# Performance work log

Measured on AMD Instinct MI355X. Metric: run time of the kernel, lower is better.

The kernel has to match this reference:

```python
import jax, jax.numpy as jnp
import numpy as np

COST_CLASS = 1.0
COST_BBOX = 5.0
COST_GIOU = 2.0


def box_cxcywh_to_xyxy(b):
    cx, cy, w, h = jnp.split(b, 4, axis=-1)
    return jnp.concatenate([cx - 0.5 * w, cy - 0.5 * h, cx + 0.5 * w, cy + 0.5 * h], axis=-1)


def generalized_box_iou(boxes1, boxes2):
    # boxes1: [N,4] xyxy, boxes2: [M,4] xyxy -> [N,M]
    area1 = (boxes1[:, 2] - boxes1[:, 0]) * (boxes1[:, 3] - boxes1[:, 1])
    area2 = (boxes2[:, 2] - boxes2[:, 0]) * (boxes2[:, 3] - boxes2[:, 1])
    lt = jnp.maximum(boxes1[:, None, :2], boxes2[None, :, :2])
    rb = jnp.minimum(boxes1[:, None, 2:], boxes2[None, :, 2:])
    wh = jnp.clip(rb - lt, 0.0)
    inter = wh[..., 0] * wh[..., 1]
    union = area1[:, None] + area2[None, :] - inter
    iou = inter / union
    lt_e = jnp.minimum(boxes1[:, None, :2], boxes2[None, :, :2])
    rb_e = jnp.maximum(boxes1[:, None, 2:], boxes2[None, :, 2:])
    wh_e = jnp.clip(rb_e - lt_e, 0.0)
    area_e = wh_e[..., 0] * wh_e[..., 1]
    return iou - (area_e - union) / area_e


def setup_inputs() -> dict:
    key = jax.random.key(0)
    k1, k2, k3, k4 = jax.random.split(key, 4)
    pred_logits = jax.random.normal(k1, (16, 900, 91), dtype=jnp.float32)
    pred_boxes = jax.random.uniform(k2, (16, 900, 4), dtype=jnp.float32)  # cxcywh in (0,1)
    tgt_labels = jax.random.randint(k3, (1600,), 0, 91)
    tgt_boxes = jax.random.uniform(k4, (1600, 4), dtype=jnp.float32)
    return {"pred_logits": pred_logits, "pred_boxes": pred_boxes,
            "tgt_labels": tgt_labels, "tgt_boxes": tgt_boxes}


def reference(pred_logits, pred_boxes, tgt_labels, tgt_boxes):
    bs, num_queries, _ = pred_logits.shape
    out_prob = jax.nn.softmax(pred_logits.reshape(bs * num_queries, -1), axis=-1)  # [BQ, C]
    out_bbox = pred_boxes.reshape(bs * num_queries, 4)  # [BQ, 4]
    # classification cost: -p(class=tgt)
    cost_class = -out_prob[:, tgt_labels]  # [BQ, M]
    # L1 cdist on cxcywh boxes
    cost_bbox = jnp.sum(jnp.abs(out_bbox[:, None, :] - tgt_boxes[None, :, :]), axis=-1)  # [BQ, M]
    # GIoU cost
    cost_giou = -generalized_box_iou(box_cxcywh_to_xyxy(out_bbox), box_cxcywh_to_xyxy(tgt_boxes))
    C = COST_BBOX * cost_bbox + COST_CLASS * cost_class + COST_GIOU * cost_giou
    return C.reshape(bs, num_queries, -1)  # [bs, Q, total_tgt]
```

## Files before the change

### kernel.cpp

```cpp
#include <hip/hip_runtime.h>

#define QT 8
#define NM 1600
#define NG (NM / 4)
#define NC 91
#define BLOCK 256

typedef float f32x4 __attribute__((ext_vector_type(4)));
typedef float f32x2 __attribute__((ext_vector_type(2)));

__global__ __launch_bounds__(BLOCK, 5) void matcher_cost_kernel(
    const float* __restrict__ logits,
    const float* __restrict__ pboxes,
    const int*   __restrict__ tlabels,
    const float* __restrict__ tboxes,
    float* __restrict__ out)
{
    __shared__ float4 s_cx[NG], s_cy[NG], s_hw[NG], s_hh[NG];
    __shared__ unsigned s_lab[NG];
    __shared__ float s_c2[QT][NC + 1];

    const int tid  = threadIdx.x;
    const int wv   = tid >> 6;
    const int lane = tid & 63;
    const int q0   = blockIdx.x * QT;

    const float4* tb4 = (const float4*)tboxes;
    const int4*   lb4 = (const int4*)tlabels;
    for (int g = tid; g < NG; g += BLOCK) {
        float4 t0 = tb4[4 * g + 0], t1 = tb4[4 * g + 1];
        float4 t2 = tb4[4 * g + 2], t3 = tb4[4 * g + 3];
        s_cx[g] = make_float4(t0.x, t1.x, t2.x, t3.x);
        s_cy[g] = make_float4(t0.y, t1.y, t2.y, t3.y);
        s_hw[g] = make_float4(0.5f * t0.z, 0.5f * t1.z, 0.5f * t2.z, 0.5f * t3.z);
        s_hh[g] = make_float4(0.5f * t0.w, 0.5f * t1.w, 0.5f * t2.w, 0.5f * t3.w);
        int4 vl = lb4[g];
        s_lab[g] = (unsigned)(vl.x & 0xff) | ((unsigned)(vl.y & 0xff) << 8)
                 | ((unsigned)(vl.z & 0xff) << 16) | ((unsigned)(vl.w & 0xff) << 24);
    }

    #pragma unroll
    for (int k = 0; k < 2; ++k) {
        const int ql = 2 * wv + k;
        const float* lrow = logits + (size_t)(q0 + ql) * NC;
        float v0 = (lane      < NC) ? lrow[lane]      : -3.4e38f;
        float v1 = (lane + 64 < NC) ? lrow[lane + 64] : -3.4e38f;
        float mx = fmaxf(v0, v1);
        #pragma unroll
        for (int off = 32; off; off >>= 1) mx = fmaxf(mx, __shfl_xor(mx, off));
        float e0 = (lane      < NC) ? __expf(v0 - mx) : 0.0f;
        float e1 = (lane + 64 < NC) ? __expf(v1 - mx) : 0.0f;
        float s = e0 + e1;
        #pragma unroll
        for (int off = 32; off; off >>= 1) s += __shfl_xor(s, off);
        float inv = 1.0f / s;
        if (lane      < NC) s_c2[ql][lane]      = 2.0f - e0 * inv;
        if (lane + 64 < NC) s_c2[ql][lane + 64] = 2.0f - e1 * inv;
    }

    f32x2 qcx[2], qcy[2], qhw[2], qhh[2], qa[2];
    #pragma unroll
    for (int k = 0; k < 2; ++k) {
        float4 pb = ((const float4*)pboxes)[q0 + 2 * wv + k];
        qcx[k] = (f32x2){pb.x, pb.x};
        qcy[k] = (f32x2){pb.y, pb.y};
        qhw[k] = (f32x2){0.5f * pb.z, 0.5f * pb.z};
        qhh[k] = (f32x2){0.5f * pb.w, 0.5f * pb.w};
        float a = pb.z * pb.w;
        qa[k]  = (f32x2){a, a};
    }

    __syncthreads();

    const f32x2 zero2 = {0.0f, 0.0f};

    for (int g = lane; g < NG; g += 64) {
        float4 vcx = s_cx[g], vcy = s_cy[g], vhw = s_hw[g], vhh = s_hh[g];
        unsigned labw = s_lab[g];
        f32x2 tcx[2] = {{vcx.x, vcx.y}, {vcx.z, vcx.w}};
        f32x2 tcy[2] = {{vcy.x, vcy.y}, {vcy.z, vcy.w}};
        f32x2 thw[2] = {{vhw.x, vhw.y}, {vhw.z, vhw.w}};
        f32x2 thh[2] = {{vhh.x, vhh.y}, {vhh.z, vhh.w}};
        f32x2 ta[2];
        #pragma unroll
        for (int h = 0; h < 2; ++h) ta[h] = 4.0f * (thw[h] * thh[h]);

        #pragma unroll
        for (int k = 0; k < 2; ++k) {
            const int ql = 2 * wv + k;
            const float* tab = s_c2[ql];
            f32x2 rr2[2];
            #pragma unroll
            for (int h = 0; h < 2; ++h) {
                f32x2 adx = __builtin_elementwise_abs(qcx[k] - tcx[h]);
                f32x2 ady = __builtin_elementwise_abs(qcy[k] - tcy[h]);
                f32x2 adw = __builtin_elementwise_abs(qhw[k] - thw[h]);
                f32x2 adh = __builtin_elementwise_abs(qhh[k] - thh[h]);
                f32x2 A = adx + ady;
                f32x2 B = adw + adh;
                f32x2 sx = qhw[k] + thw[h];
                f32x2 sy = qhh[k] + thh[h];
                f32x2 mxx = __builtin_elementwise_max(adx, adw);
                f32x2 mxy = __builtin_elementwise_max(ady, adh);
                f32x2 iw = __builtin_elementwise_max(sx - mxx, zero2);
                f32x2 ih = __builtin_elementwise_max(sy - mxy, zero2);
                f32x2 inter = iw * ih;
                f32x2 earea = (sx + mxx) * (sy + mxy);
                f32x2 uni = (qa[k] + ta[h]) - inter;
                f32x2 ue = uni * earea;
                f32x2 rr = {__builtin_amdgcn_rcpf(ue[0]),
                            __builtin_amdgcn_rcpf(ue[1])};
                f32x2 X = (uni * uni + inter * earea) * rr;
                f32x2 c2 = {tab[(labw >> (16 * h)) & 0xff],
                            tab[(labw >> (16 * h + 8)) & 0xff]};
                rr2[h] = -2.0f * X + (5.0f * A + (10.0f * B + c2));
            }
            f32x4 r4 = {rr2[0][0], rr2[0][1], rr2[1][0], rr2[1][1]};
            __builtin_nontemporal_store(r4,
                (f32x4*)(out + (size_t)(q0 + ql) * NM) + g);
        }
    }
}

extern "C" void kernel_launch(void* const* d_in, const int* in_sizes, int n_in,
                              void* d_out, int out_size, void* d_ws, size_t ws_size,
                              hipStream_t stream) {
    const float* logits  = (const float*)d_in[0];
    const float* pboxes  = (const float*)d_in[1];
    const int*   tlabels = (const int*)d_in[2];
    const float* tboxes  = (const float*)d_in[3];
    float* out = (float*)d_out;

    const int BQ = in_sizes[1] / 4;
    const int grid = BQ / QT;
    matcher_cost_kernel<<<grid, BLOCK, 0, stream>>>(logits, pboxes, tlabels, tboxes, out);
}
```

Measured before the change: 30.74 us.

## Make matcher kernel persistent, with waves striding over query-pair halves

Replaces the one-block-per-8-queries grid with a fixed 1280-block persistent grid. Each wave loops over work units made of a query pair and one half of the targets. This spreads the target-table staging in shared memory over many query rows and gives finer-grained load balancing. In exchange, each wave recomputes the softmax for its query pair once per half, so every logits row is processed twice, and there is no barrier between each wave's shared-table writes and its reads.

```diff
diff --git a/kernel.cpp b/kernel.cpp
--- a/kernel.cpp
+++ b/kernel.cpp
@@ -1,10 +1,11 @@
 #include <hip/hip_runtime.h>
 
-#define QT 8
 #define NM 1600
 #define NG (NM / 4)
+#define NH (NG / 2)
 #define NC 91
 #define BLOCK 256
+#define GRID 1280
 
 typedef float f32x4 __attribute__((ext_vector_type(4)));
 typedef float f32x2 __attribute__((ext_vector_type(2)));
@@ -14,16 +15,16 @@
     const float* __restrict__ pboxes,
     const int*   __restrict__ tlabels,
     const float* __restrict__ tboxes,
-    float* __restrict__ out)
+    float* __restrict__ out,
+    int BQ)
 {
     __shared__ float4 s_cx[NG], s_cy[NG], s_hw[NG], s_hh[NG];
     __shared__ unsigned s_lab[NG];
-    __shared__ float s_c2[QT][NC + 1];
+    __shared__ float s_tab[4][2][NC + 5];
 
     const int tid  = threadIdx.x;
     const int wv   = tid >> 6;
     const int lane = tid & 63;
-    const int q0   = blockIdx.x * QT;
 
     const float4* tb4 = (const float4*)tboxes;
     const int4*   lb4 = (const int4*)tlabels;
@@ -38,86 +39,93 @@
         s_lab[g] = (unsigned)(vl.x & 0xff) | ((unsigned)(vl.y & 0xff) << 8)
                  | ((unsigned)(vl.z & 0xff) << 16) | ((unsigned)(vl.w & 0xff) << 24);
     }
-
-    #pragma unroll
-    for (int k = 0; k < 2; ++k) {
-        const int ql = 2 * wv + k;
-        const float* lrow = logits + (size_t)(q0 + ql) * NC;
-        float v0 = (lane      < NC) ? lrow[lane]      : -3.4e38f;
-        float v1 = (lane + 64 < NC) ? lrow[lane + 64] : -3.4e38f;
-        float mx = fmaxf(v0, v1);
-        #pragma unroll
-        for (int off = 32; off; off >>= 1) mx = fmaxf(mx, __shfl_xor(mx, off));
-        float e0 = (lane      < NC) ? __expf(v0 - mx) : 0.0f;
-        float e1 = (lane + 64 < NC) ? __expf(v1 - mx) : 0.0f;
-        float s = e0 + e1;
-        #pragma unroll
-        for (int off = 32; off; off >>= 1) s += __shfl_xor(s, off);
-        float inv = 1.0f / s;
-        if (lane      < NC) s_c2[ql][lane]      = 2.0f - e0 * inv;
-        if (lane + 64 < NC) s_c2[ql][lane + 64] = 2.0f - e1 * inv;
-    }
-
-    f32x2 qcx[2], qcy[2], qhw[2], qhh[2], qa[2];
-    #pragma unroll
-    for (int k = 0; k < 2; ++k) {
-        float4 pb = ((const float4*)pboxes)[q0 + 2 * wv + k];
-        qcx[k] = (f32x2){pb.x, pb.x};
-        qcy[k] = (f32x2){pb.y, pb.y};
-        qhw[k] = (f32x2){0.5f * pb.z, 0.5f * pb.z};
-        qhh[k] = (f32x2){0.5f * pb.w, 0.5f * pb.w};
-        float a = pb.z * pb.w;
-        qa[k]  = (f32x2){a, a};
-    }
-
     __syncthreads();
 
+    const int npair = BQ >> 1;
+    const int totw  = (int)gridDim.x * 4;
+    const int gwid  = (int)blockIdx.x * 4 + wv;
     const f32x2 zero2 = {0.0f, 0.0f};
 
-    for (int g = lane; g < NG; g += 64) {
-        float4 vcx = s_cx[g], vcy = s_cy[g], vhw = s_hw[g], vhh = s_hh[g];
-        unsigned labw = s_lab[g];
-        f32x2 tcx[2] = {{vcx.x, vcx.y}, {vcx.z, vcx.w}};
-        f32x2 tcy[2] = {{vcy.x, vcy.y}, {vcy.z, vcy.w}};
-        f32x2 thw[2] = {{vhw.x, vhw.y}, {vhw.z, vhw.w}};
-        f32x2 thh[2] = {{vhh.x, vhh.y}, {vhh.z, vhh.w}};
-        f32x2 ta[2];
-        #pragma unroll
-        for (int h = 0; h < 2; ++h) ta[h] = 4.0f * (thw[h] * thh[h]);
+    for (int u = gwid; u < BQ; u += totw) {
+        const int half = (u >= npair) ? 1 : 0;
+        const int pair = u - half * npair;
 
         #pragma unroll
         for (int k = 0; k < 2; ++k) {
-            const int ql = 2 * wv + k;
-            const float* tab = s_c2[ql];
-            f32x2 rr2[2];
+            const int q = 2 * pair + k;
+            const float* lrow = logits + (size_t)q * NC;
+            float v0 = (lane      < NC) ? lrow[lane]      : -3.4e38f;
+            float v1 = (lane + 64 < NC) ? lrow[lane + 64] : -3.4e38f;
+            float mx = fmaxf(v0, v1);
             #pragma unroll
-            for (int h = 0; h < 2; ++h) {
-                f32x2 adx = __builtin_elementwise_abs(qcx[k] - tcx[h]);
-                f32x2 ady = __builtin_elementwise_abs(qcy[k] - tcy[h]);
-                f32x2 adw = __builtin_elementwise_abs(qhw[k] - thw[h]);
-                f32x2 adh = __builtin_elementwise_abs(qhh[k] - thh[h]);
-                f32x2 A = adx + ady;
-                f32x2 B = adw + adh;
-                f32x2 sx = qhw[k] + thw[h];
-                f32x2 sy = qhh[k] + thh[h];
-                f32x2 mxx = __builtin_elementwise_max(adx, adw);
-                f32x2 mxy = __builtin_elementwise_max(ady, adh);
-                f32x2 iw = __builtin_elementwise_max(sx - mxx, zero2);
-                f32x2 ih = __builtin_elementwise_max(sy - mxy, zero2);
-                f32x2 inter = iw * ih;
-                f32x2 earea = (sx + mxx) * (sy + mxy);
-                f32x2 uni = (qa[k] + ta[h]) - inter;
-                f32x2 ue = uni * earea;
-                f32x2 rr = {__builtin_amdgcn_rcpf(ue[0]),
-                            __builtin_amdgcn_rcpf(ue[1])};
-                f32x2 X = (uni * uni + inter * earea) * rr;
-                f32x2 c2 = {tab[(labw >> (16 * h)) & 0xff],
-                            tab[(labw >> (16 * h + 8)) & 0xff]};
-                rr2[h] = -2.0f * X + (5.0f * A + (10.0f * B + c2));
+            for (int off = 32; off; off >>= 1) mx = fmaxf(mx, __shfl_xor(mx, off));
+            float e0 = (lane      < NC) ? __expf(v0 - mx) : 0.0f;
+            float e1 = (lane + 64 < NC) ? __expf(v1 - mx) : 0.0f;
+            float s = e0 + e1;
+            #pragma unroll
+            for (int off = 32; off; off >>= 1) s += __shfl_xor(s, off);
+            float inv = 1.0f / s;
+            if (lane      < NC) s_tab[wv][k][lane]      = 2.0f - e0 * inv;
+            if (lane + 64 < NC) s_tab[wv][k][lane + 64] = 2.0f - e1 * inv;
+        }
+
+        f32x2 qcx[2], qcy[2], qhw[2], qhh[2], qa[2];
+        #pragma unroll
+        for (int k = 0; k < 2; ++k) {
+            float4 pb = ((const float4*)pboxes)[2 * pair + k];
+            qcx[k] = (f32x2){pb.x, pb.x};
+            qcy[k] = (f32x2){pb.y, pb.y};
+            qhw[k] = (f32x2){0.5f * pb.z, 0.5f * pb.z};
+            qhh[k] = (f32x2){0.5f * pb.w, 0.5f * pb.w};
+            float a = pb.z * pb.w;
+            qa[k]  = (f32x2){a, a};
+        }
+
+        const int gbeg = half * NH;
+        for (int g = gbeg + lane; g < gbeg + NH; g += 64) {
+            float4 vcx = s_cx[g], vcy = s_cy[g], vhw = s_hw[g], vhh = s_hh[g];
+            unsigned labw = s_lab[g];
+            f32x2 tcx[2] = {{vcx.x, vcx.y}, {vcx.z, vcx.w}};
+            f32x2 tcy[2] = {{vcy.x, vcy.y}, {vcy.z, vcy.w}};
+            f32x2 thw[2] = {{vhw.x, vhw.y}, {vhw.z, vhw.w}};
+            f32x2 thh[2] = {{vhh.x, vhh.y}, {vhh.z, vhh.w}};
+            f32x2 ta[2];
+            #pragma unroll
+            for (int h = 0; h < 2; ++h) ta[h] = 4.0f * (thw[h] * thh[h]);
+
+            #pragma unroll
+            for (int k = 0; k < 2; ++k) {
+                const float* tab = s_tab[wv][k];
+                f32x2 rr2[2];
+                #pragma unroll
+                for (int h = 0; h < 2; ++h) {
+                    f32x2 adx = __builtin_elementwise_abs(qcx[k] - tcx[h]);
+                    f32x2 ady = __builtin_elementwise_abs(qcy[k] - tcy[h]);
+                    f32x2 adw = __builtin_elementwise_abs(qhw[k] - thw[h]);
+                    f32x2 adh = __builtin_elementwise_abs(qhh[k] - thh[h]);
+                    f32x2 A = adx + ady;
+                    f32x2 B = adw + adh;
+                    f32x2 sx = qhw[k] + thw[h];
+                    f32x2 sy = qhh[k] + thh[h];
+                    f32x2 mxx = __builtin_elementwise_max(adx, adw);
+                    f32x2 mxy = __builtin_elementwise_max(ady, adh);
+                    f32x2 iw = __builtin_elementwise_max(sx - mxx, zero2);
+                    f32x2 ih = __builtin_elementwise_max(sy - mxy, zero2);
+                    f32x2 inter = iw * ih;
+                    f32x2 earea = (sx + mxx) * (sy + mxy);
+                    f32x2 uni = (qa[k] + ta[h]) - inter;
+                    f32x2 ue = uni * earea;
+                    f32x2 rr = {__builtin_amdgcn_rcpf(ue[0]),
+                                __builtin_amdgcn_rcpf(ue[1])};
+                    f32x2 X = (uni * uni + inter * earea) * rr;
+                    f32x2 c2 = {tab[(labw >> (16 * h)) & 0xff],
+                                tab[(labw >> (16 * h + 8)) & 0xff]};
+                    rr2[h] = -2.0f * X + (5.0f * A + (10.0f * B + c2));
+                }
+                f32x4 r4 = {rr2[0][0], rr2[0][1], rr2[1][0], rr2[1][1]};
+                __builtin_nontemporal_store(r4,
+                    (f32x4*)(out + (size_t)(2 * pair + k) * NM) + g);
             }
-            f32x4 r4 = {rr2[0][0], rr2[0][1], rr2[1][0], rr2[1][1]};
-            __builtin_nontemporal_store(r4,
-                (f32x4*)(out + (size_t)(q0 + ql) * NM) + g);
         }
     }
 }
@@ -132,6 +140,6 @@
     float* out = (float*)d_out;
 
     const int BQ = in_sizes[1] / 4;
-    const int grid = BQ / QT;
-    matcher_cost_kernel<<<grid, BLOCK, 0, stream>>>(logits, pboxes, tlabels, tboxes, out);
+    matcher_cost_kernel<<<GRID, BLOCK, 0, stream>>>(logits, pboxes, tlabels,
+                                                    tboxes, out, BQ);
 }
```

New measurement: 37.23 us. 21.1% more time.

## Split softmax into a pre-pass kernel and pack target boxes as fp16 in LDS

Applied to the files above, without the earlier changes.

Moves the per-query softmax into a separate kernel that writes 2-p values into the workspace, which the cost kernel then copies into shared memory. Stores the target box coordinates in shared memory as half2 instead of float4, halving that footprint, and raises the launch-bounds occupancy hint from 5 to 8. The aim is more resident waves to hide latency on the store-bound output write. In exchange it adds a second kernel launch and a workspace round-trip. The fp16 target coordinates also lose precision, which may exceed the accuracy tolerance.

```diff
diff --git a/kernel.cpp b/kernel.cpp
--- a/kernel.cpp
+++ b/kernel.cpp
@@ -1,24 +1,51 @@
 #include <hip/hip_runtime.h>
+#include <hip/hip_fp16.h>
 
 #define QT 8
 #define NM 1600
 #define NG (NM / 4)
 #define NC 91
+#define CSTRIDE 92
 #define BLOCK 256
 
 typedef float f32x4 __attribute__((ext_vector_type(4)));
 typedef float f32x2 __attribute__((ext_vector_type(2)));
 
-__global__ __launch_bounds__(BLOCK, 5) void matcher_cost_kernel(
+__global__ __launch_bounds__(BLOCK) void softmax_c2_kernel(
+    const float* __restrict__ logits, float* __restrict__ c2, int BQ)
+{
+    const int wv = threadIdx.x >> 6, lane = threadIdx.x & 63;
+    const int q  = blockIdx.x * 4 + wv;
+    if (q >= BQ) return;
+    const float* lrow = logits + (size_t)q * NC;
+    float v0 = (lane      < NC) ? lrow[lane]      : -3.4e38f;
+    float v1 = (lane + 64 < NC) ? lrow[lane + 64] : -3.4e38f;
+    float mx = fmaxf(v0, v1);
+    #pragma unroll
+    for (int off = 32; off; off >>= 1) mx = fmaxf(mx, __shfl_xor(mx, off));
+    float e0 = (lane      < NC) ? __expf(v0 - mx) : 0.0f;
+    float e1 = (lane + 64 < NC) ? __expf(v1 - mx) : 0.0f;
+    float s = e0 + e1;
+    #pragma unroll
+    for (int off = 32; off; off >>= 1) s += __shfl_xor(s, off);
+    float inv = 1.0f / s;
+    float* crow = c2 + (size_t)q * CSTRIDE;
+    if (lane      < NC) crow[lane]      = 2.0f - e0 * inv;
+    if (lane + 64 < NC) crow[lane + 64] = 2.0f - e1 * inv;
+}
+
+template <bool USE_WS>
+__global__ __launch_bounds__(BLOCK, 8) void matcher_cost_kernel(
     const float* __restrict__ logits,
     const float* __restrict__ pboxes,
     const int*   __restrict__ tlabels,
     const float* __restrict__ tboxes,
+    const float* __restrict__ c2g,
     float* __restrict__ out)
 {
-    __shared__ float4 s_cx[NG], s_cy[NG], s_hw[NG], s_hh[NG];
+    __shared__ __half2 s_cx[NG][2], s_cy[NG][2], s_hw[NG][2], s_hh[NG][2];
     __shared__ unsigned s_lab[NG];
-    __shared__ float s_c2[QT][NC + 1];
+    __shared__ float s_c2[QT * CSTRIDE];
 
     const int tid  = threadIdx.x;
     const int wv   = tid >> 6;
@@ -30,32 +57,41 @@
     for (int g = tid; g < NG; g += BLOCK) {
         float4 t0 = tb4[4 * g + 0], t1 = tb4[4 * g + 1];
         float4 t2 = tb4[4 * g + 2], t3 = tb4[4 * g + 3];
-        s_cx[g] = make_float4(t0.x, t1.x, t2.x, t3.x);
-        s_cy[g] = make_float4(t0.y, t1.y, t2.y, t3.y);
-        s_hw[g] = make_float4(0.5f * t0.z, 0.5f * t1.z, 0.5f * t2.z, 0.5f * t3.z);
-        s_hh[g] = make_float4(0.5f * t0.w, 0.5f * t1.w, 0.5f * t2.w, 0.5f * t3.w);
+        s_cx[g][0] = __floats2half2_rn(t0.x, t1.x);
+        s_cx[g][1] = __floats2half2_rn(t2.x, t3.x);
+        s_cy[g][0] = __floats2half2_rn(t0.y, t1.y);
+        s_cy[g][1] = __floats2half2_rn(t2.y, t3.y);
+        s_hw[g][0] = __floats2half2_rn(0.5f * t0.z, 0.5f * t1.z);
+        s_hw[g][1] = __floats2half2_rn(0.5f * t2.z, 0.5f * t3.z);
+        s_hh[g][0] = __floats2half2_rn(0.5f * t0.w, 0.5f * t1.w);
+        s_hh[g][1] = __floats2half2_rn(0.5f * t2.w, 0.5f * t3.w);
         int4 vl = lb4[g];
         s_lab[g] = (unsigned)(vl.x & 0xff) | ((unsigned)(vl.y & 0xff) << 8)
                  | ((unsigned)(vl.z & 0xff) << 16) | ((unsigned)(vl.w & 0xff) << 24);
     }
 
-    #pragma unroll
-    for (int k = 0; k < 2; ++k) {
-        const int ql = 2 * wv + k;
-        const float* lrow = logits + (size_t)(q0 + ql) * NC;
-        float v0 = (lane      < NC) ? lrow[lane]      : -3.4e38f;
-        float v1 = (lane + 64 < NC) ? lrow[lane + 64] : -3.4e38f;
-        float mx = fmaxf(v0, v1);
+    if (USE_WS) {
+        const float* src = c2g + (size_t)q0 * CSTRIDE;
+        for (int i = tid; i < QT * CSTRIDE; i += BLOCK) s_c2[i] = src[i];
+    } else {
         #pragma unroll
-        for (int off = 32; off; off >>= 1) mx = fmaxf(mx, __shfl_xor(mx, off));
-        float e0 = (lane      < NC) ? __expf(v0 - mx) : 0.0f;
-        float e1 = (lane + 64 < NC) ? __expf(v1 - mx) : 0.0f;
-        float s = e0 + e1;
-        #pragma unroll
-        for (int off = 32; off; off >>= 1) s += __shfl_xor(s, off);
-        float inv = 1.0f / s;
-        if (lane      < NC) s_c2[ql][lane]      = 2.0f - e0 * inv;
-        if (lane + 64 < NC) s_c2[ql][lane + 64] = 2.0f - e1 * inv;
+        for (int k = 0; k < 2; ++k) {
+            const int ql = 2 * wv + k;
+            const float* lrow = logits + (size_t)(q0 + ql) * NC;
+            float v0 = (lane      < NC) ? lrow[lane]      : -3.4e38f;
+            float v1 = (lane + 64 < NC) ? lrow[lane + 64] : -3.4e38f;
+            float mx = fmaxf(v0, v1);
+            #pragma unroll
+            for (int off = 32; off; off >>= 1) mx = fmaxf(mx, __shfl_xor(mx, off));
+            float e0 = (lane      < NC) ? __expf(v0 - mx) : 0.0f;
+            float e1 = (lane + 64 < NC) ? __expf(v1 - mx) : 0.0f;
+            float s = e0 + e1;
+            #pragma unroll
+            for (int off = 32; off; off >>= 1) s += __shfl_xor(s, off);
+            float inv = 1.0f / s;
+            if (lane      < NC) s_c2[ql * CSTRIDE + lane]      = 2.0f - e0 * inv;
+            if (lane + 64 < NC) s_c2[ql * CSTRIDE + lane + 64] = 2.0f - e1 * inv;
+        }
     }
 
     f32x2 qcx[2], qcy[2], qhw[2], qhh[2], qa[2];
@@ -75,12 +111,15 @@
     const f32x2 zero2 = {0.0f, 0.0f};
 
     for (int g = lane; g < NG; g += 64) {
-        float4 vcx = s_cx[g], vcy = s_cy[g], vhw = s_hw[g], vhh = s_hh[g];
+        float2 cx0 = __half22float2(s_cx[g][0]), cx1 = __half22float2(s_cx[g][1]);
+        float2 cy0 = __half22float2(s_cy[g][0]), cy1 = __half22float2(s_cy[g][1]);
+        float2 hw0 = __half22float2(s_hw[g][0]), hw1 = __half22float2(s_hw[g][1]);
+        float2 hh0 = __half22float2(s_hh[g][0]), hh1 = __half22float2(s_hh[g][1]);
         unsigned labw = s_lab[g];
-        f32x2 tcx[2] = {{vcx.x, vcx.y}, {vcx.z, vcx.w}};
-        f32x2 tcy[2] = {{vcy.x, vcy.y}, {vcy.z, vcy.w}};
-        f32x2 thw[2] = {{vhw.x, vhw.y}, {vhw.z, vhw.w}};
-        f32x2 thh[2] = {{vhh.x, vhh.y}, {vhh.z, vhh.w}};
+        f32x2 tcx[2] = {{cx0.x, cx0.y}, {cx1.x, cx1.y}};
+        f32x2 tcy[2] = {{cy0.x, cy0.y}, {cy1.x, cy1.y}};
+        f32x2 thw[2] = {{hw0.x, hw0.y}, {hw1.x, hw1.y}};
+        f32x2 thh[2] = {{hh0.x, hh0.y}, {hh1.x, hh1.y}};
         f32x2 ta[2];
         #pragma unroll
         for (int h = 0; h < 2; ++h) ta[h] = 4.0f * (thw[h] * thh[h]);
@@ -88,7 +127,7 @@
         #pragma unroll
         for (int k = 0; k < 2; ++k) {
             const int ql = 2 * wv + k;
-            const float* tab = s_c2[ql];
+            const float* tab = &s_c2[ql * CSTRIDE];
             f32x2 rr2[2];
             #pragma unroll
             for (int h = 0; h < 2; ++h) {
@@ -132,6 +171,15 @@
     float* out = (float*)d_out;
 
     const int BQ = in_sizes[1] / 4;
-    const int grid = BQ / QT;
-    matcher_cost_kernel<<<grid, BLOCK, 0, stream>>>(logits, pboxes, tlabels, tboxes, out);
+    const size_t need = (size_t)BQ * CSTRIDE * sizeof(float);
+
+    if (ws_size >= need) {
+        float* c2 = (float*)d_ws;
+        softmax_c2_kernel<<<(BQ + 3) / 4, BLOCK, 0, stream>>>(logits, c2, BQ);
+        matcher_cost_kernel<true><<<BQ / QT, BLOCK, 0, stream>>>(
+            logits, pboxes, tlabels, tboxes, c2, out);
+    } else {
+        matcher_cost_kernel<false><<<BQ / QT, BLOCK, 0, stream>>>(
+            logits, pboxes, tlabels, tboxes, nullptr, out);
+    }
 }
```

Measured after the change: 109.1 us. 255% more time.
